# Kernel tuning notes

Hardware: AMD Instinct MI355X
Metric: run time of the kernel (lower is better)

Reference implementation:

```python
import jax, jax.numpy as jnp
import numpy as np

TEMPERATURE = 8.0  # sqrt(d_head=64)
NEG_INF = -1e10


def setup_inputs() -> dict:
    key = jax.random.key(0)
    k1, k2, k3, k4, k5 = jax.random.split(key, 5)
    N, L, D = 65536, 20, 64   # N = n_head(2) * batch(32768)
    B = 32768
    q = jax.random.normal(k1, (N, L, D), dtype=jnp.float32)
    k = jax.random.normal(k2, (N, L, D), dtype=jnp.float32)
    v = jax.random.normal(k3, (N, L, D), dtype=jnp.float32)
    r_pri = jax.random.uniform(k4, (B, L), dtype=jnp.float32)
    mask = jax.random.randint(k5, (N, L), 0, 2).astype(bool)
    return {"q": q, "k": k, "v": v, "r_pri": r_pri, "mask": mask}


def reference(q, k, v, r_pri, mask):
    # attn scores: elementwise multiply + reduce over feature dim -> [N, L]
    attn = jnp.sum(q * k, axis=-1)
    # reweight by per-(batch, neighbor) prior, folded-head layout [H, B, L]
    B, L = r_pri.shape
    attn = (attn.reshape(-1, B, L) * r_pri / TEMPERATURE).reshape(-1, L)
    # mask then stable softmax over neighbor dim
    attn = jnp.where(mask, NEG_INF, attn)
    attn = jax.nn.softmax(attn, axis=-1)
    # dropout omitted (inference / eval mode)
    # weighted sum of values over neighbors -> [N, D]
    output = jnp.sum(attn[..., None] * v, axis=1)
    return (output, attn)
```

## Files before the change

### kernel.cpp

```cpp
#include <hip/hip_runtime.h>


namespace {
constexpr int kL = 20;
constexpr int kD = 64;
constexpr int kB = 32768;
constexpr float kNegInf = -1e10f;
constexpr float kInvTemp = 0.125f;
}

__global__ __launch_bounds__(256) void sdpa_prior_mask_kernel(
    const float* __restrict__ q,
    const float* __restrict__ k,
    const float* __restrict__ v,
    const float* __restrict__ r_pri,
    const int* __restrict__ mask,
    float* __restrict__ out,
    float* __restrict__ attn_out,
    int N)
{
    const int wave = threadIdx.x >> 6;
    const int lane = threadIdx.x & 63;
    const int n = blockIdx.x * 4 + wave;
    if (n >= N) return;

    const int sub = lane & 15;
    const int grp = lane >> 4;

    const size_t row_base = (size_t)n * kL * kD;
    const float4* qb = (const float4*)(q + row_base);
    const float4* kb = (const float4*)(k + row_base);
    const float4* vb = (const float4*)(v + row_base);
    const int b = n & (kB - 1);
    const float* rp = r_pri + (size_t)b * kL;
    const int* mk = mask + (size_t)n * kL;

    float4 qv[5], kv[5], vv[5];
#pragma unroll
    for (int c = 0; c < 5; ++c) {
        const int idx = (4 * c + grp) * 16 + sub;
        qv[c] = qb[idx];
        kv[c] = kb[idx];
        vv[c] = vb[idx];
    }
    float rpl[5];
    int mkl[5];
#pragma unroll
    for (int c = 0; c < 5; ++c) {
        const int l = 4 * c + grp;
        rpl[c] = rp[l];
        mkl[c] = mk[l];
    }

    float x[5];
#pragma unroll
    for (int c = 0; c < 5; ++c) {
        float p = qv[c].x * kv[c].x + qv[c].y * kv[c].y +
                  qv[c].z * kv[c].z + qv[c].w * kv[c].w;
        p += __shfl_xor(p, 1);
        p += __shfl_xor(p, 2);
        p += __shfl_xor(p, 4);
        p += __shfl_xor(p, 8);
        const float scaled = p * rpl[c] * kInvTemp;
        x[c] = (mkl[c] != 0) ? kNegInf : scaled;
    }

    float m = x[0];
#pragma unroll
    for (int c = 1; c < 5; ++c) m = fmaxf(m, x[c]);
    m = fmaxf(m, __shfl_xor(m, 16));
    m = fmaxf(m, __shfl_xor(m, 32));

    float w[5];
    float s = 0.f;
#pragma unroll
    for (int c = 0; c < 5; ++c) {
        w[c] = __expf(x[c] - m);
        s += w[c];
    }
    s += __shfl_xor(s, 16);
    s += __shfl_xor(s, 32);
    const float inv_s = 1.0f / s;
#pragma unroll
    for (int c = 0; c < 5; ++c) w[c] *= inv_s;

    float4 acc = {0.f, 0.f, 0.f, 0.f};
#pragma unroll
    for (int c = 0; c < 5; ++c) {
        acc.x += w[c] * vv[c].x;
        acc.y += w[c] * vv[c].y;
        acc.z += w[c] * vv[c].z;
        acc.w += w[c] * vv[c].w;
    }
    acc.x += __shfl_xor(acc.x, 16);
    acc.x += __shfl_xor(acc.x, 32);
    acc.y += __shfl_xor(acc.y, 16);
    acc.y += __shfl_xor(acc.y, 32);
    acc.z += __shfl_xor(acc.z, 16);
    acc.z += __shfl_xor(acc.z, 32);
    acc.w += __shfl_xor(acc.w, 16);
    acc.w += __shfl_xor(acc.w, 32);

    if (grp == 0) {
        ((float4*)(out + (size_t)n * kD))[sub] = acc;
    }

#pragma unroll
    for (int c = 0; c < 5; ++c) {
        if (sub == c) attn_out[(size_t)n * kL + 4 * c + grp] = w[c];
    }
}

extern "C" void kernel_launch(void* const* d_in, const int* in_sizes, int n_in,
                              void* d_out, int out_size, void* d_ws, size_t ws_size,
                              hipStream_t stream) {
    const float* q = (const float*)d_in[0];
    const float* k = (const float*)d_in[1];
    const float* v = (const float*)d_in[2];
    const float* r_pri = (const float*)d_in[3];
    const int* mask = (const int*)d_in[4];

    const int N = in_sizes[0] / (kL * kD);
    float* out = (float*)d_out;
    float* attn = out + (size_t)N * kD;

    dim3 block(256);
    dim3 grid((N + 3) / 4);
    hipLaunchKernelGGL(sdpa_prior_mask_kernel, grid, block, 0, stream,
                       q, k, v, r_pri, mask, out, attn, N);
}
```

Measured before the change: 819.0 us.

## Skip q/k/v loads for masked neighbors and software-pipeline a persistent grid-stride loop

Each wave now loads q and k rows only for unmasked neighbor positions, and v rows only for unmasked positions or when the whole row is masked. A ballot detects the all-masked case, where softmax is uniform and every v row is needed. This cuts HBM read traffic roughly in proportion to the mask density. The kernel also becomes a persistent grid-stride loop capped at 2048 blocks, double-buffering two rows per wave so the next row's loads overlap the current row's compute. The cost is higher register pressure from holding two full sets of buffers, plus more branching.

```diff
diff --git a/kernel.cpp b/kernel.cpp
--- a/kernel.cpp
+++ b/kernel.cpp
@@ -7,7 +7,101 @@
 constexpr int kB = 32768;
 constexpr float kNegInf = -1e10f;
 constexpr float kInvTemp = 0.125f;
+constexpr int kMaxBlocks = 2048;
 }
+
+
+#define META(S, n) do {                                                        \
+    const float* rp_ = r_pri + (size_t)((n) & (kB - 1)) * kL;                  \
+    const int* mk_ = mask + (size_t)(n) * kL;                                  \
+    _Pragma("unroll")                                                          \
+    for (int c = 0; c < 5; ++c) {                                              \
+        mkl##S[c] = mk_[4 * c + grp];                                          \
+        rpl##S[c] = rp_[4 * c + grp];                                          \
+    }                                                                          \
+} while (0)
+
+#define BALLOT(S) do {                                                         \
+    bool anyu_ = false;                                                        \
+    _Pragma("unroll")                                                          \
+    for (int c = 0; c < 5; ++c) anyu_ |= (mkl##S[c] == 0);                     \
+    am##S = (__ballot(anyu_) == 0ull);                                         \
+} while (0)
+
+#define QKV(S, n) do {                                                         \
+    const size_t rb_ = (size_t)(n) * (kL * kD);                                \
+    const float4* qb_ = (const float4*)(q + rb_);                              \
+    const float4* kb_ = (const float4*)(k + rb_);                              \
+    const float4* vb_ = (const float4*)(v + rb_);                              \
+    _Pragma("unroll")                                                          \
+    for (int c = 0; c < 5; ++c) {                                              \
+        qv##S[c] = make_float4(0.f, 0.f, 0.f, 0.f);                            \
+        kv##S[c] = make_float4(0.f, 0.f, 0.f, 0.f);                            \
+        vv##S[c] = make_float4(0.f, 0.f, 0.f, 0.f);                            \
+        if (mkl##S[c] == 0) {                                                  \
+            qv##S[c] = qb_[64 * c + lane];                                     \
+            kv##S[c] = kb_[64 * c + lane];                                     \
+        }                                                                      \
+        if (mkl##S[c] == 0 || am##S) {                                         \
+            vv##S[c] = vb_[64 * c + lane];                                     \
+        }                                                                      \
+    }                                                                          \
+} while (0)
+
+#define COMPUTE_STORE(S, n) do {                                               \
+    float x_[5];                                                               \
+    _Pragma("unroll")                                                          \
+    for (int c = 0; c < 5; ++c) {                                              \
+        float p_ = qv##S[c].x * kv##S[c].x + qv##S[c].y * kv##S[c].y +         \
+                   qv##S[c].z * kv##S[c].z + qv##S[c].w * kv##S[c].w;          \
+        p_ += __shfl_xor(p_, 1);                                               \
+        p_ += __shfl_xor(p_, 2);                                               \
+        p_ += __shfl_xor(p_, 4);                                               \
+        p_ += __shfl_xor(p_, 8);                                               \
+        const float sc_ = p_ * rpl##S[c] * kInvTemp;                           \
+        x_[c] = (mkl##S[c] != 0) ? kNegInf : sc_;                              \
+    }                                                                          \
+    float m_ = x_[0];                                                          \
+    _Pragma("unroll")                                                          \
+    for (int c = 1; c < 5; ++c) m_ = fmaxf(m_, x_[c]);                         \
+    m_ = fmaxf(m_, __shfl_xor(m_, 16));                                        \
+    m_ = fmaxf(m_, __shfl_xor(m_, 32));                                        \
+    float w_[5];                                                               \
+    float s_ = 0.f;                                                            \
+    _Pragma("unroll")                                                          \
+    for (int c = 0; c < 5; ++c) {                                              \
+        w_[c] = __expf(x_[c] - m_);                                            \
+        s_ += w_[c];                                                           \
+    }                                                                          \
+    s_ += __shfl_xor(s_, 16);                                                  \
+    s_ += __shfl_xor(s_, 32);                                                  \
+    const float is_ = 1.0f / s_;                                               \
+    _Pragma("unroll")                                                          \
+    for (int c = 0; c < 5; ++c) w_[c] *= is_;                                  \
+    float4 acc_ = {0.f, 0.f, 0.f, 0.f};                                       \
+    _Pragma("unroll")                                                          \
+    for (int c = 0; c < 5; ++c) {                                              \
+        acc_.x += w_[c] * vv##S[c].x;                                          \
+        acc_.y += w_[c] * vv##S[c].y;                                          \
+        acc_.z += w_[c] * vv##S[c].z;                                          \
+        acc_.w += w_[c] * vv##S[c].w;                                          \
+    }                                                                          \
+    acc_.x += __shfl_xor(acc_.x, 16);                                          \
+    acc_.x += __shfl_xor(acc_.x, 32);                                          \
+    acc_.y += __shfl_xor(acc_.y, 16);                                          \
+    acc_.y += __shfl_xor(acc_.y, 32);                                          \
+    acc_.z += __shfl_xor(acc_.z, 16);                                          \
+    acc_.z += __shfl_xor(acc_.z, 32);                                          \
+    acc_.w += __shfl_xor(acc_.w, 16);                                          \
+    acc_.w += __shfl_xor(acc_.w, 32);                                          \
+    if (grp == 0) {                                                            \
+        ((float4*)(out + (size_t)(n) * kD))[sub] = acc_;                       \
+    }                                                                          \
+    _Pragma("unroll")                                                          \
+    for (int c = 0; c < 5; ++c) {                                              \
+        if (sub == c) attn_out[(size_t)(n) * kL + 4 * c + grp] = w_[c];        \
+    }                                                                          \
+} while (0)
 
 __global__ __launch_bounds__(256) void sdpa_prior_mask_kernel(
     const float* __restrict__ q,
@@ -19,95 +113,38 @@
     float* __restrict__ attn_out,
     int N)
 {
-    const int wave = threadIdx.x >> 6;
     const int lane = threadIdx.x & 63;
-    const int n = blockIdx.x * 4 + wave;
-    if (n >= N) return;
-
+    const int wib = threadIdx.x >> 6;
+    const int gwave = blockIdx.x * 4 + wib;
+    const int W = (int)gridDim.x * 4;
     const int sub = lane & 15;
     const int grp = lane >> 4;
 
-    const size_t row_base = (size_t)n * kL * kD;
-    const float4* qb = (const float4*)(q + row_base);
-    const float4* kb = (const float4*)(k + row_base);
-    const float4* vb = (const float4*)(v + row_base);
-    const int b = n & (kB - 1);
-    const float* rp = r_pri + (size_t)b * kL;
-    const int* mk = mask + (size_t)n * kL;
+    float4 qvA[5], kvA[5], vvA[5]; float rplA[5]; int mklA[5]; bool amA = false;
+    float4 qvB[5], kvB[5], vvB[5]; float rplB[5]; int mklB[5]; bool amB = false;
+    (void)amA; (void)amB;
 
-    float4 qv[5], kv[5], vv[5];
-#pragma unroll
-    for (int c = 0; c < 5; ++c) {
-        const int idx = (4 * c + grp) * 16 + sub;
-        qv[c] = qb[idx];
-        kv[c] = kb[idx];
-        vv[c] = vb[idx];
-    }
-    float rpl[5];
-    int mkl[5];
-#pragma unroll
-    for (int c = 0; c < 5; ++c) {
-        const int l = 4 * c + grp;
-        rpl[c] = rp[l];
-        mkl[c] = mk[l];
-    }
+    int nA = gwave;
+    if (nA >= N) return;
 
-    float x[5];
-#pragma unroll
-    for (int c = 0; c < 5; ++c) {
-        float p = qv[c].x * kv[c].x + qv[c].y * kv[c].y +
-                  qv[c].z * kv[c].z + qv[c].w * kv[c].w;
-        p += __shfl_xor(p, 1);
-        p += __shfl_xor(p, 2);
-        p += __shfl_xor(p, 4);
-        p += __shfl_xor(p, 8);
-        const float scaled = p * rpl[c] * kInvTemp;
-        x[c] = (mkl[c] != 0) ? kNegInf : scaled;
-    }
+    META(A, nA);
+    BALLOT(A);
+    QKV(A, nA);
+    int nB = nA + W;
+    if (nB < N) META(B, nB);
 
-    float m = x[0];
-#pragma unroll
-    for (int c = 1; c < 5; ++c) m = fmaxf(m, x[c]);
-    m = fmaxf(m, __shfl_xor(m, 16));
-    m = fmaxf(m, __shfl_xor(m, 32));
-
-    float w[5];
-    float s = 0.f;
-#pragma unroll
-    for (int c = 0; c < 5; ++c) {
-        w[c] = __expf(x[c] - m);
-        s += w[c];
-    }
-    s += __shfl_xor(s, 16);
-    s += __shfl_xor(s, 32);
-    const float inv_s = 1.0f / s;
-#pragma unroll
-    for (int c = 0; c < 5; ++c) w[c] *= inv_s;
-
-    float4 acc = {0.f, 0.f, 0.f, 0.f};
-#pragma unroll
-    for (int c = 0; c < 5; ++c) {
-        acc.x += w[c] * vv[c].x;
-        acc.y += w[c] * vv[c].y;
-        acc.z += w[c] * vv[c].z;
-        acc.w += w[c] * vv[c].w;
-    }
-    acc.x += __shfl_xor(acc.x, 16);
-    acc.x += __shfl_xor(acc.x, 32);
-    acc.y += __shfl_xor(acc.y, 16);
-    acc.y += __shfl_xor(acc.y, 32);
-    acc.z += __shfl_xor(acc.z, 16);
-    acc.z += __shfl_xor(acc.z, 32);
-    acc.w += __shfl_xor(acc.w, 16);
-    acc.w += __shfl_xor(acc.w, 32);
-
-    if (grp == 0) {
-        ((float4*)(out + (size_t)n * kD))[sub] = acc;
-    }
-
-#pragma unroll
-    for (int c = 0; c < 5; ++c) {
-        if (sub == c) attn_out[(size_t)n * kL + 4 * c + grp] = w[c];
+    while (nA < N) {
+        const bool hasB = (nB < N);
+        if (hasB) { BALLOT(B); QKV(B, nB); }
+        COMPUTE_STORE(A, nA);
+        const int nA2 = nA + 2 * W;
+        const bool hasA2 = (nA2 < N);
+        if (hasA2) { META(A, nA2); BALLOT(A); QKV(A, nA2); }
+        if (hasB) COMPUTE_STORE(B, nB);
+        const int nB2 = nB + 2 * W;
+        if (hasA2 && nB2 < N) META(B, nB2);
+        nA = nA2;
+        nB = nB2;
     }
 }
 
@@ -124,8 +161,11 @@
     float* out = (float*)d_out;
     float* attn = out + (size_t)N * kD;
 
+    int blocks = (N + 3) / 4;
+    if (blocks > kMaxBlocks) blocks = kMaxBlocks;
+
     dim3 block(256);
-    dim3 grid((N + 3) / 4);
+    dim3 grid(blocks);
     hipLaunchKernelGGL(sdpa_prior_mask_kernel, grid, block, 0, stream,
                        q, k, v, r_pri, mask, out, attn, N);
 }
```

After: 738.8 us. 1.11x faster.

## Add persistent pipelined wave kernel with async LDS loads and masked-row load skipping

Applied to the files above, without the earlier changes.

Adds a new kernel in which each single-wave block processes 32 rows in a strided loop. It double-buffers q/k into shared memory using global_load_lds async copies with explicit vmcnt waits, and prefetches mask and prior metadata two rows ahead. Loads of q, k and v for masked neighbors are redirected to a small dummy buffer, and v is skipped unless every neighbor is masked. The goal is to cut DRAM traffic, since roughly half the neighbors are masked, and to overlap memory latency with compute. The cost is reduced occupancy from 64-thread blocks and fragile hand-counted waitcnt values.

```diff
diff --git a/kernel.cpp b/kernel.cpp
--- a/kernel.cpp
+++ b/kernel.cpp
@@ -1,4 +1,5 @@
 #include <hip/hip_runtime.h>
+#include <stdint.h>
 
 
 namespace {
@@ -7,6 +8,174 @@
 constexpr int kB = 32768;
 constexpr float kNegInf = -1e10f;
 constexpr float kInvTemp = 0.125f;
+constexpr int kRowsPerWave = 32;
+}
+
+#define AS1 __attribute__((address_space(1)))
+#define AS3 __attribute__((address_space(3)))
+
+__device__ __forceinline__ void gld_lds16(const void* gsrc, void* ldst) {
+    __builtin_amdgcn_global_load_lds((const AS1 void*)gsrc, (AS3 void*)ldst,
+                                     16, 0, 0);
+}
+
+#define WAITCNT_SB(N) do {                                                     \
+    asm volatile("s_waitcnt vmcnt(" #N ")" ::: "memory");                      \
+    __builtin_amdgcn_sched_barrier(0);                                         \
+} while (0)
+
+#define LOAD_META_TO(MK, RP, AM, n) do {                                       \
+    const int b_ = (n) & (kB - 1);                                             \
+    const float* rp_ = r_pri + (size_t)b_ * kL;                                \
+    const int* mk_ = mask + (size_t)(n) * kL;                                  \
+    _Pragma("unroll")                                                          \
+    for (int c = 0; c < 5; ++c) { MK[c] = mk_[4*c + grp]; RP[c] = rp_[4*c + grp]; } \
+    bool any_ = false;                                                         \
+    _Pragma("unroll")                                                          \
+    for (int c = 0; c < 5; ++c) any_ |= (MK[c] == 0);                          \
+    AM = (__ballot(any_) == 0ull);                                             \
+} while (0)
+
+#define ISSUE_QK(MK, n, LQ, LK) do {                                           \
+    const size_t rb_ = (size_t)(n) * (kL * kD);                                \
+    const float4* qb_ = (const float4*)(q + rb_);                              \
+    const float4* kb_ = (const float4*)(k + rb_);                              \
+    _Pragma("unroll")                                                          \
+    for (int c = 0; c < 5; ++c) {                                              \
+        const bool on_ = (MK[c] == 0);                                         \
+        const float4* qs_ = on_ ? (qb_ + 64*c + lane) : (dummy + lane);        \
+        const float4* ks_ = on_ ? (kb_ + 64*c + lane) : (dummy + lane);        \
+        gld_lds16(qs_, (LQ) + c*256);                                          \
+        gld_lds16(ks_, (LK) + c*256);                                          \
+    }                                                                          \
+} while (0)
+
+#define BODY(MK, RP, AM, LQ, LK, ncur, WLIT, DOMETA, DOISSUE) do {             \
+    const int n_ = (ncur);                                                     \
+    WAITCNT_SB(WLIT);                                                          \
+        \
+    float4 vv_[5];                                                             \
+    { const float4* vb_ = (const float4*)(v + (size_t)n_ * (kL * kD));         \
+      _Pragma("unroll")                                                        \
+      for (int c = 0; c < 5; ++c) {                                            \
+          const bool want_ = (MK[c] == 0) || AM;                               \
+          const float4* vs_ = want_ ? (vb_ + 64*c + lane) : (dummy + lane);    \
+          const float4 t_ = *vs_;                                              \
+          vv_[c].x = want_ ? t_.x : 0.f;                                       \
+          vv_[c].y = want_ ? t_.y : 0.f;                                       \
+          vv_[c].z = want_ ? t_.z : 0.f;                                       \
+          vv_[c].w = want_ ? t_.w : 0.f;                                       \
+      } }                                                                      \
+                    \
+    int mn_[5]; float rn_[5];                                                  \
+    if (DOMETA) {                                                              \
+        const int nn_ = n_ + 2 * GW;                                           \
+        const float* rp2_ = r_pri + (size_t)(nn_ & (kB - 1)) * kL;             \
+        const int* mk2_ = mask + (size_t)nn_ * kL;                             \
+        _Pragma("unroll")                                                      \
+        for (int c = 0; c < 5; ++c) { mn_[c] = mk2_[4*c + grp]; rn_[c] = rp2_[4*c + grp]; } \
+    }                                                                          \
+                                  \
+    float x_[5];                                                               \
+    { const float4* lq_ = (const float4*)(LQ);                                 \
+      const float4* lk_ = (const float4*)(LK);                                 \
+      _Pragma("unroll")                                                        \
+      for (int c = 0; c < 5; ++c) {                                            \
+          const float4 a_ = lq_[64*c + lane];                                  \
+          const float4 b2_ = lk_[64*c + lane];                                 \
+          float p_ = a_.x*b2_.x + a_.y*b2_.y + a_.z*b2_.z + a_.w*b2_.w;        \
+          p_ += __shfl_xor(p_, 1);                                             \
+          p_ += __shfl_xor(p_, 2);                                             \
+          p_ += __shfl_xor(p_, 4);                                             \
+          p_ += __shfl_xor(p_, 8);                                             \
+          x_[c] = (MK[c] != 0) ? kNegInf : (p_ * RP[c] * kInvTemp);            \
+      } }                                                                      \
+                                                        \
+    float m_ = x_[0];                                                          \
+    _Pragma("unroll")                                                          \
+    for (int c = 1; c < 5; ++c) m_ = fmaxf(m_, x_[c]);                         \
+    m_ = fmaxf(m_, __shfl_xor(m_, 16));                                        \
+    m_ = fmaxf(m_, __shfl_xor(m_, 32));                                        \
+    float w_[5]; float s_ = 0.f;                                               \
+    _Pragma("unroll")                                                          \
+    for (int c = 0; c < 5; ++c) { w_[c] = __expf(x_[c] - m_); s_ += w_[c]; }   \
+    s_ += __shfl_xor(s_, 16);                                                  \
+    s_ += __shfl_xor(s_, 32);                                                  \
+    const float is_ = 1.0f / s_;                                               \
+    _Pragma("unroll")                                                          \
+    for (int c = 0; c < 5; ++c) w_[c] *= is_;                                  \
+                                                                       \
+    float4 acc_ = {0.f, 0.f, 0.f, 0.f};                                        \
+    _Pragma("unroll")                                                          \
+    for (int c = 0; c < 5; ++c) {                                              \
+        acc_.x += w_[c] * vv_[c].x; acc_.y += w_[c] * vv_[c].y;                \
+        acc_.z += w_[c] * vv_[c].z; acc_.w += w_[c] * vv_[c].w;                \
+    }                                                                          \
+    acc_.x += __shfl_xor(acc_.x, 16); acc_.x += __shfl_xor(acc_.x, 32);        \
+    acc_.y += __shfl_xor(acc_.y, 16); acc_.y += __shfl_xor(acc_.y, 32);        \
+    acc_.z += __shfl_xor(acc_.z, 16); acc_.z += __shfl_xor(acc_.z, 32);        \
+    acc_.w += __shfl_xor(acc_.w, 16); acc_.w += __shfl_xor(acc_.w, 32);        \
+           \
+    if (grp == 0) ((float4*)(out + (size_t)n_ * kD))[sub] = acc_;              \
+    _Pragma("unroll")                                                          \
+    for (int c = 0; c < 5; ++c) {                                              \
+        if (sub == c) attn_out[(size_t)n_ * kL + 4*c + grp] = w_[c];           \
+    }                                                                          \
+                    \
+    if (DOMETA) {                                                              \
+        _Pragma("unroll")                                                      \
+        for (int c = 0; c < 5; ++c) { MK[c] = mn_[c]; RP[c] = rn_[c]; }        \
+        bool any2_ = false;                                                    \
+        _Pragma("unroll")                                                      \
+        for (int c = 0; c < 5; ++c) any2_ |= (MK[c] == 0);                     \
+        AM = (__ballot(any2_) == 0ull);                                        \
+    }                                                                          \
+    if (DOISSUE) { ISSUE_QK(MK, n_ + 2 * GW, LQ, LK); }                        \
+} while (0)
+
+__global__ __launch_bounds__(64) void sdpa_pipe_kernel(
+    const float* __restrict__ q,
+    const float* __restrict__ k,
+    const float* __restrict__ v,
+    const float* __restrict__ r_pri,
+    const int* __restrict__ mask,
+    const float4* __restrict__ dummy,
+    float* __restrict__ out,
+    float* __restrict__ attn_out,
+    int N)
+{
+    const int lane = threadIdx.x;
+    const int sub = lane & 15;
+    const int grp = lane >> 4;
+    const int g = blockIdx.x;
+    const int GW = (int)gridDim.x;
+
+    __shared__ float s_qk[2][2][kL * kD];
+    float* lq0 = &s_qk[0][0][0]; float* lk0 = &s_qk[0][1][0];
+    float* lq1 = &s_qk[1][0][0]; float* lk1 = &s_qk[1][1][0];
+
+    int mklE[5]; float rplE[5]; bool amE;
+    int mklO[5]; float rplO[5]; bool amO;
+
+    const int n0 = g;
+
+    LOAD_META_TO(mklE, rplE, amE, n0);
+    ISSUE_QK(mklE, n0, lq0, lk0);
+    LOAD_META_TO(mklO, rplO, amO, n0 + GW);
+    ISSUE_QK(mklO, n0 + GW, lq1, lk1);
+
+    int n = n0;
+    BODY(mklE, rplE, amE, lq0, lk0, n,      20, true, true);
+    BODY(mklO, rplO, amO, lq1, lk1, n + GW, 31, true, true);
+    n += 2 * GW;
+#pragma unroll 1
+    for (int it = 1; it <= kRowsPerWave / 2 - 2; ++it) {
+        BODY(mklE, rplE, amE, lq0, lk0, n,      31, true, true);
+        BODY(mklO, rplO, amO, lq1, lk1, n + GW, 31, true, true);
+        n += 2 * GW;
+    }
+    BODY(mklE, rplE, amE, lq0, lk0, n,      31, false, false);
+    BODY(mklO, rplO, amO, lq1, lk1, n + GW, 11, false, false);
 }
 
 __global__ __launch_bounds__(256) void sdpa_prior_mask_kernel(
@@ -23,7 +192,6 @@
     const int lane = threadIdx.x & 63;
     const int n = blockIdx.x * 4 + wave;
     if (n >= N) return;
-
     const int sub = lane & 15;
     const int grp = lane >> 4;
 
@@ -31,83 +199,59 @@
     const float4* qb = (const float4*)(q + row_base);
     const float4* kb = (const float4*)(k + row_base);
     const float4* vb = (const float4*)(v + row_base);
-    const int b = n & (kB - 1);
-    const float* rp = r_pri + (size_t)b * kL;
+    const float* rp = r_pri + (size_t)(n & (kB - 1)) * kL;
     const int* mk = mask + (size_t)n * kL;
 
+    float rpl[5]; int mkl[5];
+#pragma unroll
+    for (int c = 0; c < 5; ++c) { mkl[c] = mk[4*c + grp]; rpl[c] = rp[4*c + grp]; }
+    bool anyu = false;
+#pragma unroll
+    for (int c = 0; c < 5; ++c) anyu |= (mkl[c] == 0);
+    const bool am = (__ballot(anyu) == 0ull);
+
     float4 qv[5], kv[5], vv[5];
 #pragma unroll
     for (int c = 0; c < 5; ++c) {
-        const int idx = (4 * c + grp) * 16 + sub;
-        qv[c] = qb[idx];
-        kv[c] = kb[idx];
-        vv[c] = vb[idx];
-    }
-    float rpl[5];
-    int mkl[5];
-#pragma unroll
-    for (int c = 0; c < 5; ++c) {
-        const int l = 4 * c + grp;
-        rpl[c] = rp[l];
-        mkl[c] = mk[l];
-    }
-
+        qv[c] = make_float4(0.f,0.f,0.f,0.f);
+        kv[c] = make_float4(0.f,0.f,0.f,0.f);
+        vv[c] = make_float4(0.f,0.f,0.f,0.f);
+        if (mkl[c] == 0) { qv[c] = qb[64*c + lane]; kv[c] = kb[64*c + lane]; }
+        if (mkl[c] == 0 || am) vv[c] = vb[64*c + lane];
+    }
     float x[5];
 #pragma unroll
     for (int c = 0; c < 5; ++c) {
-        float p = qv[c].x * kv[c].x + qv[c].y * kv[c].y +
-                  qv[c].z * kv[c].z + qv[c].w * kv[c].w;
-        p += __shfl_xor(p, 1);
-        p += __shfl_xor(p, 2);
-        p += __shfl_xor(p, 4);
-        p += __shfl_xor(p, 8);
-        const float scaled = p * rpl[c] * kInvTemp;
-        x[c] = (mkl[c] != 0) ? kNegInf : scaled;
-    }
-
+        float p = qv[c].x*kv[c].x + qv[c].y*kv[c].y + qv[c].z*kv[c].z + qv[c].w*kv[c].w;
+        p += __shfl_xor(p, 1); p += __shfl_xor(p, 2);
+        p += __shfl_xor(p, 4); p += __shfl_xor(p, 8);
+        x[c] = (mkl[c] != 0) ? kNegInf : (p * rpl[c] * kInvTemp);
+    }
     float m = x[0];
 #pragma unroll
     for (int c = 1; c < 5; ++c) m = fmaxf(m, x[c]);
-    m = fmaxf(m, __shfl_xor(m, 16));
-    m = fmaxf(m, __shfl_xor(m, 32));
-
-    float w[5];
-    float s = 0.f;
-#pragma unroll
-    for (int c = 0; c < 5; ++c) {
-        w[c] = __expf(x[c] - m);
-        s += w[c];
-    }
-    s += __shfl_xor(s, 16);
-    s += __shfl_xor(s, 32);
+    m = fmaxf(m, __shfl_xor(m, 16)); m = fmaxf(m, __shfl_xor(m, 32));
+    float w[5]; float s = 0.f;
+#pragma unroll
+    for (int c = 0; c < 5; ++c) { w[c] = __expf(x[c] - m); s += w[c]; }
+    s += __shfl_xor(s, 16); s += __shfl_xor(s, 32);
     const float inv_s = 1.0f / s;
 #pragma unroll
     for (int c = 0; c < 5; ++c) w[c] *= inv_s;
-
-    float4 acc = {0.f, 0.f, 0.f, 0.f};
-#pragma unroll
-    for (int c = 0; c < 5; ++c) {
-        acc.x += w[c] * vv[c].x;
-        acc.y += w[c] * vv[c].y;
-        acc.z += w[c] * vv[c].z;
-        acc.w += w[c] * vv[c].w;
-    }
-    acc.x += __shfl_xor(acc.x, 16);
-    acc.x += __shfl_xor(acc.x, 32);
-    acc.y += __shfl_xor(acc.y, 16);
-    acc.y += __shfl_xor(acc.y, 32);
-    acc.z += __shfl_xor(acc.z, 16);
-    acc.z += __shfl_xor(acc.z, 32);
-    acc.w += __shfl_xor(acc.w, 16);
-    acc.w += __shfl_xor(acc.w, 32);
-
-    if (grp == 0) {
-        ((float4*)(out + (size_t)n * kD))[sub] = acc;
-    }
-
-#pragma unroll
-    for (int c = 0; c < 5; ++c) {
-        if (sub == c) attn_out[(size_t)n * kL + 4 * c + grp] = w[c];
+    float4 acc = {0.f,0.f,0.f,0.f};
+#pragma unroll
+    for (int c = 0; c < 5; ++c) {
+        acc.x += w[c]*vv[c].x; acc.y += w[c]*vv[c].y;
+        acc.z += w[c]*vv[c].z; acc.w += w[c]*vv[c].w;
+    }
+    acc.x += __shfl_xor(acc.x,16); acc.x += __shfl_xor(acc.x,32);
+    acc.y += __shfl_xor(acc.y,16); acc.y += __shfl_xor(acc.y,32);
+    acc.z += __shfl_xor(acc.z,16); acc.z += __shfl_xor(acc.z,32);
+    acc.w += __shfl_xor(acc.w,16); acc.w += __shfl_xor(acc.w,32);
+    if (grp == 0) ((float4*)(out + (size_t)n * kD))[sub] = acc;
+#pragma unroll
+    for (int c = 0; c < 5; ++c) {
+        if (sub == c) attn_out[(size_t)n * kL + 4*c + grp] = w[c];
     }
 }
 
@@ -124,8 +268,18 @@
     float* out = (float*)d_out;
     float* attn = out + (size_t)N * kD;
 
-    dim3 block(256);
-    dim3 grid((N + 3) / 4);
-    hipLaunchKernelGGL(sdpa_prior_mask_kernel, grid, block, 0, stream,
-                       q, k, v, r_pri, mask, out, attn, N);
-}
+    if (N % kRowsPerWave == 0) {
+        const float4* dummy = (d_ws != nullptr && ws_size >= 1024)
+                                  ? (const float4*)d_ws : (const float4*)q;
+        const int waves = N / kRowsPerWave;
+        dim3 block(64);
+        dim3 grid(waves);
+        hipLaunchKernelGGL(sdpa_pipe_kernel, grid, block, 0, stream,
+                           q, k, v, r_pri, mask, dummy, out, attn, N);
+    } else {
+        dim3 block(256);
+        dim3 grid((N + 3) / 4);
+        hipLaunchKernelGGL(sdpa_prior_mask_kernel, grid, block, 0, stream,
+                           q, k, v, r_pri, mask, out, attn, N);
+    }
+}
```

New measurement: 740.9 us. 9.5% less time.
